# Kernel optimization log

Measured on AMD Instinct MI355X. Metric: run time of the kernel, lower is better.

The kernel has to match this reference:

```python
import jax, jax.numpy as jnp
import numpy as np

N, M, D = 256, 64, 1024


def _l2norm(x, axis=-1, eps=1e-12):
    # tf.math.l2_normalize semantics: x / sqrt(max(sum(x^2), eps))
    sq = jnp.sum(x * x, axis=axis, keepdims=True)
    return x * jax.lax.rsqrt(jnp.maximum(sq, eps))


def setup_inputs() -> dict:
    key = jax.random.key(0)
    k1, = jax.random.split(key, 1)
    inputs = jax.random.normal(k1, (N * M, D), dtype=jnp.float32)
    w = jnp.full((1,), 10.0, dtype=jnp.float32)
    b = jnp.full((1,), -5.0, dtype=jnp.float32)
    return {"inputs": inputs, "w": w, "b": b}


def reference(inputs, w, b):
    emb = inputs.reshape(N, M, D)                       # (N, M, D)
    # speaker centroids (normalized mean over utterances)
    center = _l2norm(jnp.mean(emb, axis=1))             # (N, D)
    # leave-one-out centroid per utterance: sum over M minus self (NOT divided)
    center_except = _l2norm(jnp.sum(emb, axis=1, keepdims=True) - emb)  # (N, M, D)
    # off-diagonal similarities: every utterance vs every speaker centroid
    sim_all = jnp.einsum('jmd,id->jmi', emb, center)    # (N_utt_spk j, M, N_centroid i)
    # diagonal (i == j): utterance vs its own leave-one-out centroid
    diag = jnp.sum(center_except * emb, axis=-1)        # (N, M)
    eye = jnp.eye(N, dtype=bool)[:, None, :]            # (N, 1, N)
    sim = jnp.where(eye, diag[:, :, None], sim_all)     # (N, M, N)
    sim = w * sim + b
    return sim.reshape(N * M, N)
```

## Files before the change

kernel.cpp:

```cpp
#include <hip/hip_runtime.h>

#define NSPK 256
#define MUTT 64
#define DDIM 1024
#define NROW (NSPK * MUTT)

using frag_ab = __attribute__((ext_vector_type(8))) short;
using frag_cd = __attribute__((ext_vector_type(4))) float;

static __device__ __forceinline__ unsigned short f32_to_bf16(float f) {
    unsigned int u = __float_as_uint(f);
    return (unsigned short)((u + 0x7FFFu + ((u >> 16) & 1u)) >> 16);
}
static __device__ __forceinline__ unsigned int pack2(float a, float b) {
    return (unsigned)f32_to_bf16(a) | ((unsigned)f32_to_bf16(b) << 16);
}
static __device__ __forceinline__ void gload16(const void* g, void* l) {
    __builtin_amdgcn_global_load_lds(
        (const __attribute__((address_space(1))) unsigned int*)g,
        (__attribute__((address_space(3))) unsigned int*)l, 16, 0, 0);
}


__global__ void __launch_bounds__(256) k_prep(const float* __restrict__ emb,
                                              float* __restrict__ Sp,
                                              unsigned short* __restrict__ ebf,
                                              float* __restrict__ qg) {
    const int j = blockIdx.x;
    const int h = blockIdx.y;
    const int t = threadIdx.x;
    const int lane = t & 63, wave = t >> 6;
    const size_t rowbase = (size_t)j * MUTT + (size_t)h * 16;
    const float* src = emb + rowbase * DDIM + (size_t)t * 4;
    unsigned short* edst = ebf + rowbase * DDIM + (size_t)t * 4;
    __shared__ float qws[16][4];
    float4 s = make_float4(0.f, 0.f, 0.f, 0.f);
    #pragma unroll
    for (int m = 0; m < 16; ++m) {
        float4 v = *(const float4*)(src + (size_t)m * DDIM);
        s.x += v.x; s.y += v.y; s.z += v.z; s.w += v.w;
        float qp = v.x * v.x + v.y * v.y + v.z * v.z + v.w * v.w;
        #pragma unroll
        for (int off = 32; off > 0; off >>= 1) qp += __shfl_down(qp, off, 64);
        if (lane == 0) qws[m][wave] = qp;
        *(uint2*)(edst + (size_t)m * DDIM) = make_uint2(pack2(v.x, v.y), pack2(v.z, v.w));
    }
    __syncthreads();
    if (t < 16) qg[rowbase + t] = qws[t][0] + qws[t][1] + qws[t][2] + qws[t][3];
    *(float4*)(Sp + ((size_t)h * NSPK + j) * DDIM + (size_t)t * 4) = s;
}

template <int P>
__global__ void k_center(const float* __restrict__ Sp, unsigned short* __restrict__ cbf,
                         float* __restrict__ normS2g, float* __restrict__ normSg) {
    const int j = blockIdx.x;
    const int t = threadIdx.x;
    float4 v = make_float4(0.f, 0.f, 0.f, 0.f);
    #pragma unroll
    for (int p = 0; p < P; ++p) {
        float4 a = *(const float4*)(Sp + ((size_t)p * NSPK + j) * DDIM + (size_t)t * 4);
        v.x += a.x; v.y += a.y; v.z += a.z; v.w += a.w;
    }
    float sq = v.x * v.x + v.y * v.y + v.z * v.z + v.w * v.w;
    #pragma unroll
    for (int off = 32; off > 0; off >>= 1) sq += __shfl_down(sq, off, 64);
    __shared__ float ws[4];
    __shared__ float sc_sh;
    const int lane = t & 63, wave = t >> 6;
    if (lane == 0) ws[wave] = sq;
    __syncthreads();
    if (t == 0) {
        float tot = ws[0] + ws[1] + ws[2] + ws[3];
        normS2g[j] = tot;
        normSg[j]  = sqrtf(tot);
        float msq = tot * (1.0f / 4096.0f);
        sc_sh = rsqrtf(fmaxf(msq, 1e-12f)) * (1.0f / 64.0f);
    }
    __syncthreads();
    const float sc = sc_sh;
    *(uint2*)(cbf + (size_t)j * DDIM + (size_t)t * 4) =
        make_uint2(pack2(v.x * sc, v.y * sc), pack2(v.z * sc, v.w * sc));
}

#define BK 64
__global__ void __launch_bounds__(256, 5)
k_gemm4(const unsigned short* __restrict__ ebf, const unsigned short* __restrict__ cbf,
        const float* __restrict__ qg, const float* __restrict__ n2g,
        const float* __restrict__ n1g,
        const float* __restrict__ wp, const float* __restrict__ bp,
        float* __restrict__ out) {
    __shared__ unsigned short lds[2 * 8192];

    const int tid = threadIdx.x, lane = tid & 63, wave = tid >> 6;
    const int rt = blockIdx.x;
    const int ct = blockIdx.y;
    const int row0 = rt * 64;
    const int c0 = ct * 64;
    const int jspk = rt;

    int goff[2];
    #pragma unroll
    for (int i = 0; i < 2; ++i) {
        int c = i * 256 + tid, row = c >> 3, sw = c & 7;
        goff[i] = row * (DDIM * 2) + ((sw ^ (row & 7)) << 4);
    }
    const int stbase = wave * 512;
    const char* agbase = (const char*)(ebf + (size_t)row0 * DDIM);
    const char* bgbase = (const char*)(cbf + (size_t)c0 * DDIM);

    const int quad = lane >> 4;
    const int m16 = lane & 15;
    const int wrow = wave >> 1, wcol = wave & 1;
    int arow[2], brow[2];
    #pragma unroll
    for (int rr = 0; rr < 2; ++rr) arow[rr] = wrow * 32 + rr * 16 + m16;
    #pragma unroll
    for (int cc = 0; cc < 2; ++cc) brow[cc] = wcol * 32 + cc * 16 + m16;

    frag_cd acc[2][2];
    #pragma unroll
    for (int rr = 0; rr < 2; ++rr)
        #pragma unroll
        for (int cc = 0; cc < 2; ++cc) acc[rr][cc] = (frag_cd){0.f, 0.f, 0.f, 0.f};

    auto stage = [&](int buf, int kt) {
        const char* ag = agbase + (size_t)kt * BK * 2;
        const char* bg = bgbase + (size_t)kt * BK * 2;
        unsigned short* Ld = &lds[buf * 8192];
        #pragma unroll
        for (int i = 0; i < 2; ++i) {
            gload16(ag + goff[i], Ld + i * 2048 + stbase);
            gload16(bg + goff[i], Ld + 4096 + i * 2048 + stbase);
        }
    };

    stage(0, 0);
    stage(1, 1);

    const int NIT = DDIM / BK;
    for (int it = 0; it < NIT; ++it) {
        if (it < NIT - 1) asm volatile("s_waitcnt vmcnt(4)" ::: "memory");
        else              asm volatile("s_waitcnt vmcnt(0)" ::: "memory");
        __builtin_amdgcn_s_barrier();
        __builtin_amdgcn_sched_barrier(0);

        const unsigned short* L = &lds[(it & 1) * 8192];
        #pragma unroll
        for (int s = 0; s < 2; ++s) {
            frag_ab af[2], bf[2];
            const int kc = (s << 2) + quad;
            #pragma unroll
            for (int rr = 0; rr < 2; ++rr) {
                int addr = arow[rr] * 128 + ((kc ^ (arow[rr] & 7)) << 4);
                af[rr] = *(const frag_ab*)&L[addr >> 1];
            }
            #pragma unroll
            for (int cc = 0; cc < 2; ++cc) {
                int addr = 8192 + brow[cc] * 128 + ((kc ^ (brow[cc] & 7)) << 4);
                bf[cc] = *(const frag_ab*)&L[addr >> 1];
            }
            #pragma unroll
            for (int rr = 0; rr < 2; ++rr)
                #pragma unroll
                for (int cc = 0; cc < 2; ++cc)
                    acc[rr][cc] = __builtin_amdgcn_mfma_f32_16x16x32_bf16(
                        af[rr], bf[cc], acc[rr][cc], 0, 0, 0);
        }

        __builtin_amdgcn_s_barrier();
        __builtin_amdgcn_sched_barrier(0);
        if (it + 2 < NIT) stage(it & 1, it + 2);
    }

    const float wv = wp[0], bv = bp[0];
    const float ns2 = n2g[jspk], ns = n1g[jspk];
    #pragma unroll
    for (int rr = 0; rr < 2; ++rr) {
        int rbase = wrow * 32 + rr * 16 + (quad << 2);
        #pragma unroll
        for (int cc = 0; cc < 2; ++cc) {
            int col = c0 + wcol * 32 + cc * 16 + m16;
            frag_cd v = acc[rr][cc];
            #pragma unroll
            for (int r2 = 0; r2 < 4; ++r2) {
                int grow = row0 + rbase + r2;
                float val = v[r2];
                if (col == jspk) {
                    float q = qg[grow];
                    float rd = val * ns;
                    float den2 = ns2 - 2.f * rd + q;
                    val = (rd - q) * rsqrtf(fmaxf(den2, 1e-12f));
                }
                out[(size_t)grow * NSPK + col] = wv * val + bv;
            }
        }
    }
}


__global__ void k_sums(const float* __restrict__ emb, float* __restrict__ Sp) {
    const int j = blockIdx.x;
    const int h = blockIdx.y;
    const int c = threadIdx.x;
    const float* base = emb + ((size_t)j * MUTT + (size_t)h * 32) * DDIM + (size_t)c * 4;
    float4 acc = make_float4(0.f, 0.f, 0.f, 0.f);
    #pragma unroll 8
    for (int m = 0; m < 32; ++m) {
        float4 v = *(const float4*)(base + (size_t)m * DDIM);
        acc.x += v.x; acc.y += v.y; acc.z += v.z; acc.w += v.w;
    }
    *(float4*)(Sp + ((size_t)h * NSPK + j) * DDIM + (size_t)c * 4) = acc;
}

__global__ void __launch_bounds__(256)
k_gemm_old(const float* __restrict__ emb, const unsigned short* __restrict__ cbf,
           const float* __restrict__ normS2g, const float* __restrict__ normSg,
           const float* __restrict__ wp, const float* __restrict__ bp,
           float* __restrict__ out) {
    __shared__ unsigned short Asm[32][32];
    __shared__ unsigned short Bsm[256][32];
    __shared__ float qpart[32][8];
    __shared__ float qfin[32];
    const int tid = threadIdx.x, lane = tid & 63, wave = tid >> 6;
    const int row0 = blockIdx.x * 32;
    const int jspk = row0 >> 6;
    frag_cd acc[2][4];
    #pragma unroll
    for (int rr = 0; rr < 2; ++rr)
        #pragma unroll
        for (int cc = 0; cc < 4; ++cc) acc[rr][cc] = (frag_cd){0.f, 0.f, 0.f, 0.f};
    const int ar = tid >> 3, ak = (tid & 7) << 2;
    const float* aptr = emb + (size_t)(row0 + ar) * DDIM + ak;
    float qacc = 0.f;
    const int bi = tid >> 2, bk = (tid & 3) << 3;
    const int am = lane & 15, kq = (lane >> 4) << 3;
    for (int k0 = 0; k0 < DDIM; k0 += 32) {
        __syncthreads();
        float4 av = *(const float4*)(aptr + k0);
        qacc += av.x * av.x + av.y * av.y + av.z * av.z + av.w * av.w;
        *(uint2*)&Asm[ar][ak] = make_uint2(pack2(av.x, av.y), pack2(av.z, av.w));
        #pragma unroll
        for (int p = 0; p < 4; ++p) {
            int brow = p * 64 + bi;
            *(uint4*)&Bsm[brow][bk] = *(const uint4*)(cbf + (size_t)brow * DDIM + k0 + bk);
        }
        __syncthreads();
        frag_ab afr[2], bfr[4];
        #pragma unroll
        for (int rr = 0; rr < 2; ++rr) afr[rr] = *(const frag_ab*)&Asm[rr * 16 + am][kq];
        #pragma unroll
        for (int cc = 0; cc < 4; ++cc) bfr[cc] = *(const frag_ab*)&Bsm[wave * 64 + cc * 16 + am][kq];
        #pragma unroll
        for (int rr = 0; rr < 2; ++rr)
            #pragma unroll
            for (int cc = 0; cc < 4; ++cc)
                acc[rr][cc] = __builtin_amdgcn_mfma_f32_16x16x32_bf16(afr[rr], bfr[cc], acc[rr][cc], 0, 0, 0);
    }
    qpart[ar][tid & 7] = qacc;
    __syncthreads();
    if (tid < 32) {
        float s = 0.f;
        #pragma unroll
        for (int u = 0; u < 8; ++u) s += qpart[tid][u];
        qfin[tid] = s;
    }
    __syncthreads();
    const float wv = wp[0], bv = bp[0];
    const float ns2 = normS2g[jspk], ns = normSg[jspk];
    #pragma unroll
    for (int rr = 0; rr < 2; ++rr) {
        int rbase = rr * 16 + ((lane >> 4) << 2);
        #pragma unroll
        for (int cc = 0; cc < 4; ++cc) {
            int col = wave * 64 + cc * 16 + (lane & 15);
            frag_cd v = acc[rr][cc];
            #pragma unroll
            for (int r2 = 0; r2 < 4; ++r2) {
                int lrow = rbase + r2;
                float val = v[r2];
                if (col == jspk) {
                    float q = qfin[lrow];
                    float rd = val * ns;
                    float den2 = ns2 - 2.f * rd + q;
                    val = (rd - q) * rsqrtf(fmaxf(den2, 1e-12f));
                }
                out[(size_t)(row0 + lrow) * NSPK + col] = wv * val + bv;
            }
        }
    }
}

extern "C" void kernel_launch(void* const* d_in, const int* in_sizes, int n_in,
                              void* d_out, int out_size, void* d_ws, size_t ws_size,
                              hipStream_t stream) {
    const float* emb = (const float*)d_in[0];
    const float* w   = (const float*)d_in[1];
    const float* b   = (const float*)d_in[2];
    float* out = (float*)d_out;

    const size_t sz_Sp  = (size_t)4 * NSPK * DDIM * 4;
    const size_t sz_ebf = (size_t)NROW * DDIM * 2;
    const size_t sz_cbf = (size_t)NSPK * DDIM * 2;
    const size_t sz_qg  = (size_t)NROW * 4;
    const size_t need = sz_Sp + sz_ebf + sz_cbf + sz_qg + 2 * NSPK * 4;

    if (ws_size >= need) {
        char* p = (char*)d_ws;
        float* Sp = (float*)p;                    p += sz_Sp;
        unsigned short* ebf = (unsigned short*)p; p += sz_ebf;
        unsigned short* cbf = (unsigned short*)p; p += sz_cbf;
        float* qg = (float*)p;                    p += sz_qg;
        float* n2 = (float*)p;
        float* n1 = n2 + NSPK;
        k_prep<<<dim3(NSPK, 4), 256, 0, stream>>>(emb, Sp, ebf, qg);
        k_center<4><<<NSPK, 256, 0, stream>>>(Sp, cbf, n2, n1);
        k_gemm4<<<dim3(NSPK, 4), 256, 0, stream>>>(ebf, cbf, qg, n2, n1, w, b, out);
    } else {
        float* Sp = (float*)d_ws;
        unsigned short* cbf = (unsigned short*)(Sp + 2 * NSPK * DDIM);
        float* n2 = (float*)(cbf + NSPK * DDIM);
        float* n1 = n2 + NSPK;
        k_sums<<<dim3(NSPK, 2), 256, 0, stream>>>(emb, Sp);
        k_center<2><<<NSPK, 256, 0, stream>>>(Sp, cbf, n2, n1);
        k_gemm_old<<<NROW / 32, 256, 0, stream>>>(emb, cbf, n2, n1, w, b, out);
    }
}
```

Measured before the change: 127.5 us.

## Fuse prep and center kernels; convert fp32 embeddings to bf16 inside GEMM

Merges the prep and centroid kernels into one kernel per speaker, so the partial-sum buffer and one launch go away. The bf16 copy of the embeddings is no longer written. The GEMM now loads fp32 rows into registers, converts them to bf16, and writes them to LDS with software prefetch one K-step ahead. This removes a 32 MB bf16 write plus its 32 MB re-read, but each of the 4 column-tile blocks now reads 64 MB of fp32 A data instead of bf16. It also uses full __syncthreads and lowers the occupancy hint from 5 to 4.

```diff
diff --git a/kernel.cpp b/kernel.cpp
--- a/kernel.cpp
+++ b/kernel.cpp
@@ -22,69 +22,62 @@
 }
 
 
-__global__ void __launch_bounds__(256) k_prep(const float* __restrict__ emb,
-                                              float* __restrict__ Sp,
-                                              unsigned short* __restrict__ ebf,
-                                              float* __restrict__ qg) {
+__global__ void __launch_bounds__(512) k_prepc(const float* __restrict__ emb,
+                                               unsigned short* __restrict__ cbf,
+                                               float* __restrict__ qg,
+                                               float* __restrict__ n2g,
+                                               float* __restrict__ n1g) {
     const int j = blockIdx.x;
-    const int h = blockIdx.y;
     const int t = threadIdx.x;
+    const int cg = t & 255;
+    const int half = t >> 8;
     const int lane = t & 63, wave = t >> 6;
-    const size_t rowbase = (size_t)j * MUTT + (size_t)h * 16;
-    const float* src = emb + rowbase * DDIM + (size_t)t * 4;
-    unsigned short* edst = ebf + rowbase * DDIM + (size_t)t * 4;
-    __shared__ float qws[16][4];
+    const size_t rb = (size_t)j * MUTT + (size_t)half * 32;
+    const float* src = emb + rb * DDIM + (size_t)cg * 4;
+    __shared__ float qws[64][4];
+    __shared__ float4 csum[256];
+    __shared__ float red[4];
+    __shared__ float sc_sh;
     float4 s = make_float4(0.f, 0.f, 0.f, 0.f);
-    #pragma unroll
-    for (int m = 0; m < 16; ++m) {
+    #pragma unroll 8
+    for (int m = 0; m < 32; ++m) {
         float4 v = *(const float4*)(src + (size_t)m * DDIM);
         s.x += v.x; s.y += v.y; s.z += v.z; s.w += v.w;
         float qp = v.x * v.x + v.y * v.y + v.z * v.z + v.w * v.w;
         #pragma unroll
         for (int off = 32; off > 0; off >>= 1) qp += __shfl_down(qp, off, 64);
-        if (lane == 0) qws[m][wave] = qp;
-        *(uint2*)(edst + (size_t)m * DDIM) = make_uint2(pack2(v.x, v.y), pack2(v.z, v.w));
-    }
-    __syncthreads();
-    if (t < 16) qg[rowbase + t] = qws[t][0] + qws[t][1] + qws[t][2] + qws[t][3];
-    *(float4*)(Sp + ((size_t)h * NSPK + j) * DDIM + (size_t)t * 4) = s;
-}
-
-template <int P>
-__global__ void k_center(const float* __restrict__ Sp, unsigned short* __restrict__ cbf,
-                         float* __restrict__ normS2g, float* __restrict__ normSg) {
-    const int j = blockIdx.x;
-    const int t = threadIdx.x;
-    float4 v = make_float4(0.f, 0.f, 0.f, 0.f);
-    #pragma unroll
-    for (int p = 0; p < P; ++p) {
-        float4 a = *(const float4*)(Sp + ((size_t)p * NSPK + j) * DDIM + (size_t)t * 4);
-        v.x += a.x; v.y += a.y; v.z += a.z; v.w += a.w;
-    }
-    float sq = v.x * v.x + v.y * v.y + v.z * v.z + v.w * v.w;
-    #pragma unroll
-    for (int off = 32; off > 0; off >>= 1) sq += __shfl_down(sq, off, 64);
-    __shared__ float ws[4];
-    __shared__ float sc_sh;
-    const int lane = t & 63, wave = t >> 6;
-    if (lane == 0) ws[wave] = sq;
+        if (lane == 0) qws[half * 32 + m][wave & 3] = qp;
+    }
+    if (half) csum[cg] = s;
+    __syncthreads();
+    if (t < 64) qg[(size_t)j * MUTT + t] = qws[t][0] + qws[t][1] + qws[t][2] + qws[t][3];
+    if (!half) {
+        float4 c = csum[cg];
+        s.x += c.x; s.y += c.y; s.z += c.z; s.w += c.w;
+        float sq = s.x * s.x + s.y * s.y + s.z * s.z + s.w * s.w;
+        #pragma unroll
+        for (int off = 32; off > 0; off >>= 1) sq += __shfl_down(sq, off, 64);
+        if (lane == 0) red[wave] = sq;
+    }
     __syncthreads();
     if (t == 0) {
-        float tot = ws[0] + ws[1] + ws[2] + ws[3];
-        normS2g[j] = tot;
-        normSg[j]  = sqrtf(tot);
+        float tot = red[0] + red[1] + red[2] + red[3];
+        n2g[j] = tot;
+        n1g[j] = sqrtf(tot);
         float msq = tot * (1.0f / 4096.0f);
         sc_sh = rsqrtf(fmaxf(msq, 1e-12f)) * (1.0f / 64.0f);
     }
     __syncthreads();
-    const float sc = sc_sh;
-    *(uint2*)(cbf + (size_t)j * DDIM + (size_t)t * 4) =
-        make_uint2(pack2(v.x * sc, v.y * sc), pack2(v.z * sc, v.w * sc));
+    if (!half) {
+        const float sc = sc_sh;
+        *(uint2*)(cbf + (size_t)j * DDIM + (size_t)cg * 4) =
+            make_uint2(pack2(s.x * sc, s.y * sc), pack2(s.z * sc, s.w * sc));
+    }
 }
 
 #define BK 64
-__global__ void __launch_bounds__(256, 5)
-k_gemm4(const unsigned short* __restrict__ ebf, const unsigned short* __restrict__ cbf,
+__global__ void __launch_bounds__(256, 4)
+k_gemmr(const float* __restrict__ emb, const unsigned short* __restrict__ cbf,
         const float* __restrict__ qg, const float* __restrict__ n2g,
         const float* __restrict__ n1g,
         const float* __restrict__ wp, const float* __restrict__ bp,
@@ -98,14 +91,20 @@
     const int c0 = ct * 64;
     const int jspk = rt;
 
-    int goff[2];
+    const int ar0 = tid >> 3, sw0 = tid & 7;
+    const int g0 = sw0 ^ (ar0 & 7);
+    const float* apg0 = emb + (size_t)(row0 + ar0) * DDIM + g0 * 8;
+    const float* apg1 = apg0 + (size_t)32 * DDIM;
+    const int alds0 = ar0 * 64 + sw0 * 8;
+    const int alds1 = alds0 + 32 * 64;
+
+    int boff[2];
     #pragma unroll
     for (int i = 0; i < 2; ++i) {
         int c = i * 256 + tid, row = c >> 3, sw = c & 7;
-        goff[i] = row * (DDIM * 2) + ((sw ^ (row & 7)) << 4);
+        boff[i] = row * (DDIM * 2) + ((sw ^ (row & 7)) << 4);
     }
     const int stbase = wave * 512;
-    const char* agbase = (const char*)(ebf + (size_t)row0 * DDIM);
     const char* bgbase = (const char*)(cbf + (size_t)c0 * DDIM);
 
     const int quad = lane >> 4;
@@ -123,28 +122,42 @@
         #pragma unroll
         for (int cc = 0; cc < 2; ++cc) acc[rr][cc] = (frag_cd){0.f, 0.f, 0.f, 0.f};
 
-    auto stage = [&](int buf, int kt) {
-        const char* ag = agbase + (size_t)kt * BK * 2;
+    float4 rA[4];
+
+    auto issueA = [&](int kt) {
+        const int ko = kt * BK;
+        rA[0] = *(const float4*)(apg0 + ko);
+        rA[1] = *(const float4*)(apg0 + ko + 4);
+        rA[2] = *(const float4*)(apg1 + ko);
+        rA[3] = *(const float4*)(apg1 + ko + 4);
+    };
+    auto writeA = [&](int buf) {
+        unsigned short* LA = &lds[buf * 8192];
+        *(uint4*)&LA[alds0] = make_uint4(pack2(rA[0].x, rA[0].y), pack2(rA[0].z, rA[0].w),
+                                         pack2(rA[1].x, rA[1].y), pack2(rA[1].z, rA[1].w));
+        *(uint4*)&LA[alds1] = make_uint4(pack2(rA[2].x, rA[2].y), pack2(rA[2].z, rA[2].w),
+                                         pack2(rA[3].x, rA[3].y), pack2(rA[3].z, rA[3].w));
+    };
+    auto stageB = [&](int buf, int kt) {
         const char* bg = bgbase + (size_t)kt * BK * 2;
-        unsigned short* Ld = &lds[buf * 8192];
-        #pragma unroll
-        for (int i = 0; i < 2; ++i) {
-            gload16(ag + goff[i], Ld + i * 2048 + stbase);
-            gload16(bg + goff[i], Ld + 4096 + i * 2048 + stbase);
-        }
+        unsigned short* Ld = &lds[buf * 8192 + 4096];
+        #pragma unroll
+        for (int i = 0; i < 2; ++i)
+            gload16(bg + boff[i], Ld + i * 2048 + stbase);
     };
 
-    stage(0, 0);
-    stage(1, 1);
+    issueA(0);
+    stageB(0, 0);
+    stageB(1, 1);
+    writeA(0);
+    __syncthreads();
 
     const int NIT = DDIM / BK;
-    for (int it = 0; it < NIT; ++it) {
-        if (it < NIT - 1) asm volatile("s_waitcnt vmcnt(4)" ::: "memory");
-        else              asm volatile("s_waitcnt vmcnt(0)" ::: "memory");
-        __builtin_amdgcn_s_barrier();
-        __builtin_amdgcn_sched_barrier(0);
-
-        const unsigned short* L = &lds[(it & 1) * 8192];
+    #pragma unroll
+    for (int t = 0; t < NIT; ++t) {
+        if (t + 1 < NIT) issueA(t + 1);
+
+        const unsigned short* L = &lds[(t & 1) * 8192];
         #pragma unroll
         for (int s = 0; s < 2; ++s) {
             frag_ab af[2], bf[2];
@@ -167,9 +180,9 @@
                         af[rr], bf[cc], acc[rr][cc], 0, 0, 0);
         }
 
-        __builtin_amdgcn_s_barrier();
-        __builtin_amdgcn_sched_barrier(0);
-        if (it + 2 < NIT) stage(it & 1, it + 2);
+        if (t + 1 < NIT) writeA((t + 1) & 1);
+        __syncthreads();
+        if (t + 2 < NIT) stageB(t & 1, t + 2);
     }
 
     const float wv = wp[0], bv = bp[0];
@@ -210,6 +223,38 @@
         acc.x += v.x; acc.y += v.y; acc.z += v.z; acc.w += v.w;
     }
     *(float4*)(Sp + ((size_t)h * NSPK + j) * DDIM + (size_t)c * 4) = acc;
+}
+
+template <int P>
+__global__ void k_center(const float* __restrict__ Sp, unsigned short* __restrict__ cbf,
+                         float* __restrict__ normS2g, float* __restrict__ normSg) {
+    const int j = blockIdx.x;
+    const int t = threadIdx.x;
+    float4 v = make_float4(0.f, 0.f, 0.f, 0.f);
+    #pragma unroll
+    for (int p = 0; p < P; ++p) {
+        float4 a = *(const float4*)(Sp + ((size_t)p * NSPK + j) * DDIM + (size_t)t * 4);
+        v.x += a.x; v.y += a.y; v.z += a.z; v.w += a.w;
+    }
+    float sq = v.x * v.x + v.y * v.y + v.z * v.z + v.w * v.w;
+    #pragma unroll
+    for (int off = 32; off > 0; off >>= 1) sq += __shfl_down(sq, off, 64);
+    __shared__ float ws[4];
+    __shared__ float sc_sh;
+    const int lane = t & 63, wave = t >> 6;
+    if (lane == 0) ws[wave] = sq;
+    __syncthreads();
+    if (t == 0) {
+        float tot = ws[0] + ws[1] + ws[2] + ws[3];
+        normS2g[j] = tot;
+        normSg[j]  = sqrtf(tot);
+        float msq = tot * (1.0f / 4096.0f);
+        sc_sh = rsqrtf(fmaxf(msq, 1e-12f)) * (1.0f / 64.0f);
+    }
+    __syncthreads();
+    const float sc = sc_sh;
+    *(uint2*)(cbf + (size_t)j * DDIM + (size_t)t * 4) =
+        make_uint2(pack2(v.x * sc, v.y * sc), pack2(v.z * sc, v.w * sc));
 }
 
 __global__ void __launch_bounds__(256)
@@ -298,23 +343,18 @@
     const float* b   = (const float*)d_in[2];
     float* out = (float*)d_out;
 
-    const size_t sz_Sp  = (size_t)4 * NSPK * DDIM * 4;
-    const size_t sz_ebf = (size_t)NROW * DDIM * 2;
     const size_t sz_cbf = (size_t)NSPK * DDIM * 2;
     const size_t sz_qg  = (size_t)NROW * 4;
-    const size_t need = sz_Sp + sz_ebf + sz_cbf + sz_qg + 2 * NSPK * 4;
+    const size_t need = sz_cbf + sz_qg + 2 * NSPK * 4;
 
     if (ws_size >= need) {
         char* p = (char*)d_ws;
-        float* Sp = (float*)p;                    p += sz_Sp;
-        unsigned short* ebf = (unsigned short*)p; p += sz_ebf;
         unsigned short* cbf = (unsigned short*)p; p += sz_cbf;
         float* qg = (float*)p;                    p += sz_qg;
         float* n2 = (float*)p;
         float* n1 = n2 + NSPK;
-        k_prep<<<dim3(NSPK, 4), 256, 0, stream>>>(emb, Sp, ebf, qg);
-        k_center<4><<<NSPK, 256, 0, stream>>>(Sp, cbf, n2, n1);
-        k_gemm4<<<dim3(NSPK, 4), 256, 0, stream>>>(ebf, cbf, qg, n2, n1, w, b, out);
+        k_prepc<<<NSPK, 512, 0, stream>>>(emb, cbf, qg, n2, n1);
+        k_gemmr<<<dim3(NSPK, 4), 256, 0, stream>>>(emb, cbf, qg, n2, n1, w, b, out);
     } else {
         float* Sp = (float*)d_ws;
         unsigned short* cbf = (unsigned short*)(Sp + 2 * NSPK * DDIM);
```

Measured after the change: 141.6 us. 11.1% more time.
